# Kernel optimization log

Hardware: AMD Instinct MI355X
Metric: run time of the kernel (lower is better)

The kernel has to match this reference:

```python
import jax, jax.numpy as jnp
import numpy as np

NUM_HEADS = 8
LN_EPS = 1e-5


def setup_inputs() -> dict:
    key = jax.random.key(0)
    ks = jax.random.split(key, 5)
    B, C, H, W = 4, 256, 48, 48
    scale = 1.0 / np.sqrt(C)
    return {
        "x": jax.random.normal(ks[0], (B, C, H, W), dtype=jnp.float32),
        "Wq": jax.random.normal(ks[1], (C, C), dtype=jnp.float32) * scale,
        "Wk": jax.random.normal(ks[2], (C, C), dtype=jnp.float32) * scale,
        "Wv": jax.random.normal(ks[3], (C, C), dtype=jnp.float32) * scale,
        "Wo": jax.random.normal(ks[4], (C, C), dtype=jnp.float32) * scale,
        "gamma": jnp.ones((C,), dtype=jnp.float32),
        "beta": jnp.zeros((C,), dtype=jnp.float32),
    }


def reference(x, Wq, Wk, Wv, Wo, gamma, beta):
    B, C, H, W = x.shape
    hd = C // NUM_HEADS
    N = H * W
    xf = x.reshape(B, C, N)  # [B, C, N]
    # 1x1 conv (no bias) == channel matmul, then split heads: [B, h, d, N]
    def proj(Wm):
        return jnp.einsum('oc,bcn->bon', Wm, xf).reshape(B, NUM_HEADS, hd, N)
    q = proj(Wq)
    k = proj(Wk)
    v = proj(Wv)
    # scores[b,h,i,j] = sum_d q[b,h,d,i] k[b,h,d,j] / sqrt(hd)
    scores = jnp.einsum('bhdi,bhdj->bhij', q, k) / jnp.sqrt(jnp.float32(hd))
    attn = jax.nn.softmax(scores, axis=-1)  # [B, h, N, N]
    # attended[b,h,d,i] = sum_j v[b,h,d,j] attn[b,h,i,j]
    attended = jnp.einsum('bhdj,bhij->bhdi', v, attn).reshape(B, C, H, W)
    out = jnp.einsum('oc,bchw->bohw', Wo, attended) + x
    # LayerNorm over channels (applied in NHWC layout in original)
    mu = out.mean(axis=1, keepdims=True)
    var = out.var(axis=1, keepdims=True)
    out = (out - mu) * jax.lax.rsqrt(var + LN_EPS)
    out = out * gamma[None, :, None, None] + beta[None, :, None, None]
    return out
```

## Files before the change

kernel.cpp:

```cpp
#include <hip/hip_runtime.h>

#define DEVI __device__ __forceinline__

typedef __bf16 bf16x8 __attribute__((ext_vector_type(8)));
typedef float f32x4 __attribute__((ext_vector_type(4)));

#define QSCALE 0.25503488f

DEVI unsigned short bfbits(float f) {
  union { __bf16 h; unsigned short u; } x;
  x.h = (__bf16)f;
  return x.u;
}
DEVI unsigned packbf2(float a, float b) {
  return (unsigned)bfbits(a) | ((unsigned)bfbits(b) << 16);
}
DEVI float bflo(unsigned u) { return __uint_as_float(u << 16); }
DEVI float bfhi(unsigned u) { return __uint_as_float(u & 0xffff0000u); }

DEVI void gload16(const unsigned short* g, void* l) {
  __builtin_amdgcn_global_load_lds((__attribute__((address_space(1))) const unsigned*)g,
                                   (__attribute__((address_space(3))) unsigned*)l, 16, 0, 0);
}

__global__ __launch_bounds__(256) void k_prep_x(const float* __restrict__ x,
                                                unsigned short* __restrict__ xT) {
  __shared__ float tile[64][65];
  const int b = blockIdx.x, n0 = blockIdx.y * 64, c0 = blockIdx.z * 64;
  const int t = threadIdx.x, tn = t & 63, tg = t >> 6;
  const float* xp = x + ((size_t)b * 256 + c0) * 2304 + n0;
#pragma unroll
  for (int i = 0; i < 16; ++i) {
    const int c = tg * 16 + i;
    tile[c][tn] = xp[(size_t)c * 2304 + tn];
  }
  __syncthreads();
  unsigned short* op = xT + ((size_t)b * 2304 + n0) * 256 + c0;
#pragma unroll
  for (int i = 0; i < 16; ++i) {
    const int n = tg * 16 + i;
    op[(size_t)n * 256 + tn] = bfbits(tile[tn][n]);
  }
}

__global__ __launch_bounds__(256) void k_prep_w(const float* __restrict__ Wq,
                                                const float* __restrict__ Wk,
                                                const float* __restrict__ Wv,
                                                const float* __restrict__ Wo,
                                                unsigned short* __restrict__ dst) {
  const float* src = blockIdx.y == 0 ? Wq : blockIdx.y == 1 ? Wk : blockIdx.y == 2 ? Wv : Wo;
  unsigned short* d = dst + (size_t)blockIdx.y * 65536;
  const int i = (blockIdx.x * 256 + threadIdx.x) * 4;
  const float4 v = *(const float4*)(src + i);
  uint2 u;
  u.x = packbf2(v.x, v.y);
  u.y = packbf2(v.z, v.w);
  *(uint2*)(d + i) = u;
}

__global__ __launch_bounds__(256) void k_proj_qk(const unsigned short* __restrict__ xT,
                                                 const unsigned short* __restrict__ Wb,
                                                 unsigned short* __restrict__ qT,
                                                 unsigned short* __restrict__ kT) {
  const unsigned short* W = Wb + (blockIdx.z ? 65536 : 0);
  unsigned short* outp = blockIdx.z ? kT : qT;
  const float scale = blockIdx.z ? 1.0f : QSCALE;
  const int l = threadIdx.x & 63, w = threadIdx.x >> 6;
  const int lr = l & 15, lg = l >> 4;
  const int row0 = blockIdx.x * 128 + w * 32;
  const int col0 = blockIdx.y * 32;
  f32x4 acc[2][2];
#pragma unroll
  for (int i = 0; i < 2; ++i)
#pragma unroll
    for (int j = 0; j < 2; ++j) acc[i][j] = (f32x4){0.f, 0.f, 0.f, 0.f};
  for (int ks = 0; ks < 8; ++ks) {
    const int c = ks * 32 + lg * 8;
    bf16x8 a[2], bfr[2];
#pragma unroll
    for (int nt = 0; nt < 2; ++nt)
      a[nt] = *(const bf16x8*)(xT + (size_t)(row0 + nt * 16 + lr) * 256 + c);
#pragma unroll
    for (int ot = 0; ot < 2; ++ot)
      bfr[ot] = *(const bf16x8*)(W + (size_t)(col0 + ot * 16 + lr) * 256 + c);
#pragma unroll
    for (int nt = 0; nt < 2; ++nt)
#pragma unroll
      for (int ot = 0; ot < 2; ++ot)
        acc[nt][ot] = __builtin_amdgcn_mfma_f32_16x16x32_bf16(a[nt], bfr[ot], acc[nt][ot], 0, 0, 0);
  }
#pragma unroll
  for (int nt = 0; nt < 2; ++nt)
#pragma unroll
    for (int ot = 0; ot < 2; ++ot)
#pragma unroll
      for (int r = 0; r < 4; ++r) {
        const int n = row0 + nt * 16 + lg * 4 + r;
        const int o = col0 + ot * 16 + lr;
        outp[(size_t)n * 256 + o] = bfbits(acc[nt][ot][r] * scale);
      }
}

__global__ __launch_bounds__(256) void k_proj_v(const unsigned short* __restrict__ xT,
                                                const unsigned short* __restrict__ Wv,
                                                unsigned short* __restrict__ vN) {
  const int l = threadIdx.x & 63, w = threadIdx.x >> 6;
  const int lr = l & 15, lg = l >> 4;
  const int row0 = blockIdx.x * 64 + w * 16;
  const int col0 = blockIdx.y * 32;
  f32x4 acc[2];
  acc[0] = (f32x4){0.f, 0.f, 0.f, 0.f};
  acc[1] = (f32x4){0.f, 0.f, 0.f, 0.f};
  for (int ks = 0; ks < 8; ++ks) {
    const int c = ks * 32 + lg * 8;
    bf16x8 a, bfr[2];
    a = *(const bf16x8*)(Wv + (size_t)(row0 + lr) * 256 + c);
#pragma unroll
    for (int nt = 0; nt < 2; ++nt)
      bfr[nt] = *(const bf16x8*)(xT + (size_t)(col0 + nt * 16 + lr) * 256 + c);
#pragma unroll
    for (int nt = 0; nt < 2; ++nt)
      acc[nt] = __builtin_amdgcn_mfma_f32_16x16x32_bf16(a, bfr[nt], acc[nt], 0, 0, 0);
  }
  const int b = blockIdx.y / 72, nb = (blockIdx.y % 72) * 32;
#pragma unroll
  for (int nt = 0; nt < 2; ++nt)
#pragma unroll
    for (int r = 0; r < 4; ++r) {
      const int o = row0 + lg * 4 + r;
      const int n = nb + nt * 16 + lr;
      vN[(size_t)b * 589824 + (size_t)o * 2304 + n] = bfbits(acc[nt][r]);
    }
}

template <bool DIRECT>
__global__ __launch_bounds__(256) void k_attn(const unsigned short* __restrict__ qT,
                                              const unsigned short* __restrict__ kT,
                                              const unsigned short* __restrict__ vN,
                                              unsigned short* __restrict__ partO,
                                              float* __restrict__ partS,
                                              unsigned short* __restrict__ attT,
                                              int tpc) {
  __shared__ __align__(16) unsigned char sm[32768];
  const int l = threadIdx.x & 63, w = threadIdx.x >> 6;
  const int lr = l & 15, lg = l >> 4;
  const int bh = blockIdx.y, b = bh >> 3, h = bh & 7;
  const int i0 = blockIdx.x * 128 + w * 32;
  const int c = blockIdx.z, t0 = c * tpc;
  unsigned char* smw = sm + w * 4096;

  bf16x8 qf[2];
#pragma unroll
  for (int it = 0; it < 2; ++it)
    qf[it] = *(const bf16x8*)(qT + (size_t)(b * 2304 + i0 + it * 16 + lr) * 256 + h * 32 + lg * 8);

  bf16x8 ones;
#pragma unroll
  for (int e = 0; e < 8; ++e) ones[e] = (__bf16)1.0f;

  f32x4 oacc[2][2];
#pragma unroll
  for (int i = 0; i < 2; ++i)
#pragma unroll
    for (int j = 0; j < 2; ++j) oacc[i][j] = (f32x4){0.f, 0.f, 0.f, 0.f};
  f32x4 psum[2];
  psum[0] = (f32x4){0.f, 0.f, 0.f, 0.f};
  psum[1] = (f32x4){0.f, 0.f, 0.f, 0.f};

  const unsigned short* ksrc = kT + (size_t)(b * 2304 + l) * 256 + h * 32 + w * 8;
  const int vks = w >> 1;
  const int vlg = (w * 2 + (l >> 5)) & 3;
  const unsigned short* vsrc = vN + (size_t)(b * 256 + h * 32 + (l & 31)) * 2304 + vks * 32 + vlg * 8;
  const int kdst = 16384 + w * 1024;
  const int vdst = 24576 + w * 1024;

  gload16(ksrc + (size_t)t0 * 16384, sm + kdst);
  gload16(vsrc + t0 * 64, sm + vdst);
  __syncthreads();

  for (int tt = 0; tt < tpc; ++tt) {
    const int buf = tt & 1;
    if (tt < tpc - 1) {
      const int nbuf = (tt + 1) & 1;
      gload16(ksrc + (size_t)(t0 + tt + 1) * 16384, sm + kdst + nbuf * 4096);
      gload16(vsrc + (t0 + tt + 1) * 64, sm + vdst + nbuf * 4096);
    }

    const unsigned char* kb = sm + 16384 + buf * 4096;
    const unsigned char* vb = sm + 24576 + buf * 4096;

    bf16x8 kf[4];
#pragma unroll
    for (int jt = 0; jt < 4; ++jt)
      kf[jt] = *(const bf16x8*)(kb + lg * 1024 + (jt * 16 + lr) * 16);

    f32x4 s[4][2];
    const f32x4 zf = (f32x4){0.f, 0.f, 0.f, 0.f};
#pragma unroll
    for (int jt = 0; jt < 4; ++jt)
#pragma unroll
      for (int it = 0; it < 2; ++it)
        s[jt][it] = __builtin_amdgcn_mfma_f32_16x16x32_bf16(kf[jt], qf[it], zf, 0, 0, 0);

#pragma unroll
    for (int it = 0; it < 2; ++it) {
      const int iloc = it * 16 + lr;
      const unsigned swz = (unsigned)((iloc & 7) << 4);
      unsigned char* prow = smw + iloc * 128;
#pragma unroll
      for (int jt = 0; jt < 4; ++jt) {
        const float p0 = exp2f(s[jt][it][0]);
        const float p1 = exp2f(s[jt][it][1]);
        const float p2 = exp2f(s[jt][it][2]);
        const float p3 = exp2f(s[jt][it][3]);
        const unsigned jb = (unsigned)(jt * 32 + lg * 8);
        *(unsigned*)(prow + (jb ^ swz)) = packbf2(p0, p1);
        *(unsigned*)(prow + ((jb + 4) ^ swz)) = packbf2(p2, p3);
      }
    }

    bf16x8 vf[2][2], pf[2][2];
#pragma unroll
    for (int dt = 0; dt < 2; ++dt)
#pragma unroll
      for (int ks = 0; ks < 2; ++ks)
        vf[dt][ks] = *(const bf16x8*)(vb + ks * 2048 + lg * 512 + (dt * 16 + lr) * 16);
#pragma unroll
    for (int it = 0; it < 2; ++it) {
      const int iloc = it * 16 + lr;
      const unsigned swz = (unsigned)((iloc & 7) << 4);
#pragma unroll
      for (int ks = 0; ks < 2; ++ks)
        pf[it][ks] = *(const bf16x8*)(smw + iloc * 128 + ((unsigned)(ks * 64 + lg * 16) ^ swz));
    }
#pragma unroll
    for (int dt = 0; dt < 2; ++dt)
#pragma unroll
      for (int it = 0; it < 2; ++it) {
        oacc[dt][it] = __builtin_amdgcn_mfma_f32_16x16x32_bf16(vf[dt][0], pf[it][0], oacc[dt][it], 0, 0, 0);
        oacc[dt][it] = __builtin_amdgcn_mfma_f32_16x16x32_bf16(vf[dt][1], pf[it][1], oacc[dt][it], 0, 0, 0);
      }
#pragma unroll
    for (int it = 0; it < 2; ++it) {
      psum[it] = __builtin_amdgcn_mfma_f32_16x16x32_bf16(ones, pf[it][0], psum[it], 0, 0, 0);
      psum[it] = __builtin_amdgcn_mfma_f32_16x16x32_bf16(ones, pf[it][1], psum[it], 0, 0, 0);
    }
    __syncthreads();
  }

  if (DIRECT) {
#pragma unroll
    for (int it = 0; it < 2; ++it) {
      const float inv = 1.0f / psum[it][0];
      const int iloc = it * 16 + lr;
      unsigned char* orow = smw + iloc * 68;
#pragma unroll
      for (int dt = 0; dt < 2; ++dt) {
        const int d = dt * 16 + lg * 4;
        *(unsigned*)(orow + d * 2) = packbf2(oacc[dt][it][0] * inv, oacc[dt][it][1] * inv);
        *(unsigned*)(orow + d * 2 + 4) = packbf2(oacc[dt][it][2] * inv, oacc[dt][it][3] * inv);
      }
    }
    __syncthreads();
    unsigned* attu = (unsigned*)attT;
#pragma unroll
    for (int it2 = 0; it2 < 8; ++it2) {
      const int lin = it2 * 64 + l;
      const int row = lin >> 4, k = lin & 15;
      const unsigned u = *(const unsigned*)(smw + row * 68 + k * 4);
      attu[(size_t)(b * 2304 + i0 + row) * 128 + h * 16 + k] = u;
    }
  } else {
    const size_t pbase = ((size_t)(c * 32 + bh) * 2304 + i0) * 32;
#pragma unroll
    for (int it = 0; it < 2; ++it)
#pragma unroll
      for (int dt = 0; dt < 2; ++dt) {
        const size_t addr = pbase + (size_t)(it * 16 + lr) * 32 + dt * 16 + lg * 4;
        uint2 u;
        u.x = packbf2(oacc[dt][it][0], oacc[dt][it][1]);
        u.y = packbf2(oacc[dt][it][2], oacc[dt][it][3]);
        *(uint2*)(partO + addr) = u;
      }
    if (lg == 0) {
      const size_t sbase = (size_t)(c * 32 + bh) * 2304 + i0;
      partS[sbase + lr] = psum[0][0];
      partS[sbase + 16 + lr] = psum[1][0];
    }
  }
}

__global__ __launch_bounds__(256) void k_combine(const unsigned short* __restrict__ partO,
                                                 const float* __restrict__ partS,
                                                 unsigned short* __restrict__ attT,
                                                 int nc) {
  const int bid = blockIdx.x;
  const int bh = bid / 36, i0 = (bid % 36) * 64;
  const int b = bh >> 3, h = bh & 7;
  const int tid = threadIdx.x;
  const int dq = tid & 3, di = tid >> 2;
  const int i = i0 + di;

  float ssum = 0.f;
  for (int c = 0; c < nc; ++c) ssum += partS[(size_t)(c * 32 + bh) * 2304 + i];
  const float inv = 1.0f / ssum;

  float acc[8];
#pragma unroll
  for (int e = 0; e < 8; ++e) acc[e] = 0.f;
  for (int c = 0; c < nc; ++c) {
    const uint4 v = *(const uint4*)(partO + (((size_t)(c * 32 + bh) * 2304 + i) * 32 + dq * 8));
    acc[0] += bflo(v.x); acc[1] += bfhi(v.x);
    acc[2] += bflo(v.y); acc[3] += bfhi(v.y);
    acc[4] += bflo(v.z); acc[5] += bfhi(v.z);
    acc[6] += bflo(v.w); acc[7] += bfhi(v.w);
  }
  uint4 o;
  o.x = packbf2(acc[0] * inv, acc[1] * inv);
  o.y = packbf2(acc[2] * inv, acc[3] * inv);
  o.z = packbf2(acc[4] * inv, acc[5] * inv);
  o.w = packbf2(acc[6] * inv, acc[7] * inv);
  unsigned* attu = (unsigned*)attT;
  *(uint4*)(attu + (size_t)(b * 2304 + i) * 128 + h * 16 + dq * 4) = o;
}

__global__ __launch_bounds__(256) void k_out_ln(const unsigned short* __restrict__ Wo,
                                                const unsigned short* __restrict__ attT,
                                                const float* __restrict__ x,
                                                const float* __restrict__ gamma,
                                                const float* __restrict__ beta,
                                                float* __restrict__ out) {
  __shared__ float wsum[4][16], wsq[4][16], smean[16], srstd[16];
  const int l = threadIdx.x & 63, w = threadIdx.x >> 6;
  const int lr = l & 15, lg = l >> 4;
  const int b = blockIdx.x / 144;
  const int n0 = (blockIdx.x % 144) * 16;
  const int row0 = w * 64;
  const size_t bn0 = (size_t)b * 2304 + n0;

  f32x4 acc[4];
#pragma unroll
  for (int i = 0; i < 4; ++i) acc[i] = (f32x4){0.f, 0.f, 0.f, 0.f};
  for (int ks = 0; ks < 8; ++ks) {
    const int c = ks * 32 + lg * 8;
    bf16x8 a[4], bb;
#pragma unroll
    for (int rt = 0; rt < 4; ++rt)
      a[rt] = *(const bf16x8*)(Wo + (size_t)(row0 + rt * 16 + lr) * 256 + c);
    bb = *(const bf16x8*)(attT + (bn0 + lr) * 256 + c);
#pragma unroll
    for (int rt = 0; rt < 4; ++rt)
      acc[rt] = __builtin_amdgcn_mfma_f32_16x16x32_bf16(a[rt], bb, acc[rt], 0, 0, 0);
  }
  const float* xb = x + (size_t)b * 589824;
  float vals[4][4];
  float s0 = 0.f, q0 = 0.f;
#pragma unroll
  for (int rt = 0; rt < 4; ++rt)
#pragma unroll
    for (int r = 0; r < 4; ++r) {
      const int o = row0 + rt * 16 + lg * 4 + r;
      const int n = n0 + lr;
      const float vv = acc[rt][r] + xb[(size_t)o * 2304 + n];
      vals[rt][r] = vv;
      s0 += vv;
      q0 += vv * vv;
    }
  s0 += __shfl_xor(s0, 16); s0 += __shfl_xor(s0, 32);
  q0 += __shfl_xor(q0, 16); q0 += __shfl_xor(q0, 32);
  if (l < 16) {
    wsum[w][l] = s0;
    wsq[w][l] = q0;
  }
  __syncthreads();
  if (threadIdx.x < 16) {
    const int c16 = threadIdx.x;
    const float S = wsum[0][c16] + wsum[1][c16] + wsum[2][c16] + wsum[3][c16];
    const float Q = wsq[0][c16] + wsq[1][c16] + wsq[2][c16] + wsq[3][c16];
    const float mean = S * (1.0f / 256.0f);
    const float var = Q * (1.0f / 256.0f) - mean * mean;
    smean[c16] = mean;
    srstd[c16] = rsqrtf(var + 1e-5f);
  }
  __syncthreads();
  {
    const float mean = smean[lr];
    const float rstd = srstd[lr];
    const int n = n0 + lr;
#pragma unroll
    for (int rt = 0; rt < 4; ++rt)
#pragma unroll
      for (int r = 0; r < 4; ++r) {
        const int o = row0 + rt * 16 + lg * 4 + r;
        out[(size_t)b * 589824 + (size_t)o * 2304 + n] =
            (vals[rt][r] - mean) * rstd * gamma[o] + beta[o];
      }
  }
}

extern "C" void kernel_launch(void* const* d_in, const int* in_sizes, int n_in,
                              void* d_out, int out_size, void* d_ws, size_t ws_size,
                              hipStream_t stream) {
  (void)in_sizes; (void)n_in; (void)out_size;
  const float* x = (const float*)d_in[0];
  const float* Wq = (const float*)d_in[1];
  const float* Wk = (const float*)d_in[2];
  const float* Wv = (const float*)d_in[3];
  const float* Wo = (const float*)d_in[4];
  const float* gamma = (const float*)d_in[5];
  const float* beta = (const float*)d_in[6];
  float* out = (float*)d_out;
  char* ws = (char*)d_ws;
  unsigned short* attT = (unsigned short*)(ws);
  unsigned short* Wb = (unsigned short*)(ws + 4718592);
  unsigned short* qT = (unsigned short*)(ws + 5242880);
  unsigned short* kT = (unsigned short*)(ws + 9961472);
  unsigned short* vN = (unsigned short*)(ws + 14680064);
  unsigned short* xT = (unsigned short*)(ws + 19398656);

  const size_t base = 19398656;
  const size_t need4 = base + 4ull * (4718592 + 294912);
  const size_t need2 = base + 2ull * (4718592 + 294912);
  const int nc = (ws_size >= need4) ? 4 : (ws_size >= need2) ? 2 : 1;
  unsigned short* partO = (unsigned short*)(ws + base);
  float* partS = (float*)(ws + base + (size_t)nc * 4718592);

  k_prep_x<<<dim3(4, 36, 4), 256, 0, stream>>>(x, xT);
  k_prep_w<<<dim3(64, 4), 256, 0, stream>>>(Wq, Wk, Wv, Wo, Wb);
  k_proj_qk<<<dim3(72, 8, 2), 256, 0, stream>>>(xT, Wb, qT, kT);
  k_proj_v<<<dim3(4, 288), 256, 0, stream>>>(xT, Wb + 2 * 65536, vN);
  if (nc > 1) {
    k_attn<false><<<dim3(18, 32, nc), 256, 0, stream>>>(qT, kT, vN, partO, partS, attT, 36 / nc);
    k_combine<<<dim3(1152), 256, 0, stream>>>(partO, partS, attT, nc);
  } else {
    k_attn<true><<<dim3(18, 32, 1), 256, 0, stream>>>(qT, kT, vN, attT, (float*)attT, attT, 36);
  }
  k_out_ln<<<dim3(576), 256, 0, stream>>>(Wb + 3 * 65536, attT, x, gamma, beta, out);
}
```

Measured before the change: 193.6 us.

## Stage shared operands in swizzled LDS and use native exp2 in attention

Three projection/output kernels now stage the block-shared operand (W tile for q/k and v projections, attention tile for output projection) into XOR-swizzled LDS once, so waves stop re-reading it from global memory in the k-loop. The attention softmax switches to the hardware exp2 builtin, and the two 32-bit P stores are merged into one 64-bit LDS store. The cost is extra LDS use, a barrier per block, and slightly lower exp2 accuracy.

New measurement: 168.4 us. 13.0% less time.

```diff
diff --git a/kernel.cpp b/kernel.cpp
--- a/kernel.cpp
+++ b/kernel.cpp
@@ -6,6 +6,12 @@
 typedef float f32x4 __attribute__((ext_vector_type(4)));
 
 #define QSCALE 0.25503488f
+
+#if __has_builtin(__builtin_amdgcn_exp2f)
+#define EXP2(x) __builtin_amdgcn_exp2f(x)
+#else
+#define EXP2(x) __expf(0.69314718055994531f * (x))
+#endif
 
 DEVI unsigned short bfbits(float f) {
   union { __bf16 h; unsigned short u; } x;
@@ -62,6 +68,7 @@
                                                  const unsigned short* __restrict__ Wb,
                                                  unsigned short* __restrict__ qT,
                                                  unsigned short* __restrict__ kT) {
+  __shared__ __align__(16) unsigned char wlds[16384];
   const unsigned short* W = Wb + (blockIdx.z ? 65536 : 0);
   unsigned short* outp = blockIdx.z ? kT : qT;
   const float scale = blockIdx.z ? 1.0f : QSCALE;
@@ -69,6 +76,19 @@
   const int lr = l & 15, lg = l >> 4;
   const int row0 = blockIdx.x * 128 + w * 32;
   const int col0 = blockIdx.y * 32;
+  {
+    const int t = threadIdx.x;
+    const int row = t >> 3;
+    const int cj0 = (t & 7) * 4;
+#pragma unroll
+    for (int i = 0; i < 4; ++i) {
+      const int cj = cj0 + i;
+      const uint4 v = *(const uint4*)(W + (size_t)(col0 + row) * 256 + cj * 8);
+      *(uint4*)(wlds + row * 512 + ((cj * 16) ^ ((row & 7) << 4))) = v;
+    }
+  }
+  __syncthreads();
+
   f32x4 acc[2][2];
 #pragma unroll
   for (int i = 0; i < 2; ++i)
@@ -81,8 +101,10 @@
     for (int nt = 0; nt < 2; ++nt)
       a[nt] = *(const bf16x8*)(xT + (size_t)(row0 + nt * 16 + lr) * 256 + c);
 #pragma unroll
-    for (int ot = 0; ot < 2; ++ot)
-      bfr[ot] = *(const bf16x8*)(W + (size_t)(col0 + ot * 16 + lr) * 256 + c);
+    for (int ot = 0; ot < 2; ++ot) {
+      const int brow = ot * 16 + lr;
+      bfr[ot] = *(const bf16x8*)(wlds + brow * 512 + (((ks * 4 + lg) * 16) ^ ((brow & 7) << 4)));
+    }
 #pragma unroll
     for (int nt = 0; nt < 2; ++nt)
 #pragma unroll
@@ -104,17 +126,32 @@
 __global__ __launch_bounds__(256) void k_proj_v(const unsigned short* __restrict__ xT,
                                                 const unsigned short* __restrict__ Wv,
                                                 unsigned short* __restrict__ vN) {
+  __shared__ __align__(16) unsigned char wlds[32768];
   const int l = threadIdx.x & 63, w = threadIdx.x >> 6;
   const int lr = l & 15, lg = l >> 4;
-  const int row0 = blockIdx.x * 64 + w * 16;
+  const int rowbase = blockIdx.x * 64;
   const int col0 = blockIdx.y * 32;
+  {
+    const int t = threadIdx.x;
+    const int row = t >> 2;
+    const int cj0 = (t & 3) * 8;
+#pragma unroll
+    for (int i = 0; i < 8; ++i) {
+      const int cj = cj0 + i;
+      const uint4 v = *(const uint4*)(Wv + (size_t)(rowbase + row) * 256 + cj * 8);
+      *(uint4*)(wlds + row * 512 + ((cj * 16) ^ ((row & 7) << 4))) = v;
+    }
+  }
+  __syncthreads();
+
   f32x4 acc[2];
   acc[0] = (f32x4){0.f, 0.f, 0.f, 0.f};
   acc[1] = (f32x4){0.f, 0.f, 0.f, 0.f};
   for (int ks = 0; ks < 8; ++ks) {
     const int c = ks * 32 + lg * 8;
     bf16x8 a, bfr[2];
-    a = *(const bf16x8*)(Wv + (size_t)(row0 + lr) * 256 + c);
+    const int arow = w * 16 + lr;
+    a = *(const bf16x8*)(wlds + arow * 512 + (((ks * 4 + lg) * 16) ^ ((arow & 7) << 4)));
 #pragma unroll
     for (int nt = 0; nt < 2; ++nt)
       bfr[nt] = *(const bf16x8*)(xT + (size_t)(col0 + nt * 16 + lr) * 256 + c);
@@ -127,7 +164,7 @@
   for (int nt = 0; nt < 2; ++nt)
 #pragma unroll
     for (int r = 0; r < 4; ++r) {
-      const int o = row0 + lg * 4 + r;
+      const int o = rowbase + w * 16 + lg * 4 + r;
       const int n = nb + nt * 16 + lr;
       vN[(size_t)b * 589824 + (size_t)o * 2304 + n] = bfbits(acc[nt][r]);
     }
@@ -209,13 +246,15 @@
       unsigned char* prow = smw + iloc * 128;
 #pragma unroll
       for (int jt = 0; jt < 4; ++jt) {
-        const float p0 = exp2f(s[jt][it][0]);
-        const float p1 = exp2f(s[jt][it][1]);
-        const float p2 = exp2f(s[jt][it][2]);
-        const float p3 = exp2f(s[jt][it][3]);
+        const float p0 = EXP2(s[jt][it][0]);
+        const float p1 = EXP2(s[jt][it][1]);
+        const float p2 = EXP2(s[jt][it][2]);
+        const float p3 = EXP2(s[jt][it][3]);
         const unsigned jb = (unsigned)(jt * 32 + lg * 8);
-        *(unsigned*)(prow + (jb ^ swz)) = packbf2(p0, p1);
-        *(unsigned*)(prow + ((jb + 4) ^ swz)) = packbf2(p2, p3);
+        uint2 u;
+        u.x = packbf2(p0, p1);
+        u.y = packbf2(p2, p3);
+        *(uint2*)(prow + (jb ^ swz)) = u;
       }
     }
 
@@ -330,6 +369,7 @@
                                                 const float* __restrict__ gamma,
                                                 const float* __restrict__ beta,
                                                 float* __restrict__ out) {
+  __shared__ __align__(16) unsigned char alds[8192];
   __shared__ float wsum[4][16], wsq[4][16], smean[16], srstd[16];
   const int l = threadIdx.x & 63, w = threadIdx.x >> 6;
   const int lr = l & 15, lg = l >> 4;
@@ -337,6 +377,18 @@
   const int n0 = (blockIdx.x % 144) * 16;
   const int row0 = w * 64;
   const size_t bn0 = (size_t)b * 2304 + n0;
+  {
+    const int t = threadIdx.x;
+    const int row = t >> 4;
+    const int cj0 = (t & 15) * 2;
+#pragma unroll
+    for (int i = 0; i < 2; ++i) {
+      const int cj = cj0 + i;
+      const uint4 v = *(const uint4*)(attT + (bn0 + row) * 256 + cj * 8);
+      *(uint4*)(alds + row * 512 + ((cj * 16) ^ ((row & 7) << 4))) = v;
+    }
+  }
+  __syncthreads();
 
   f32x4 acc[4];
 #pragma unroll
@@ -347,7 +399,7 @@
 #pragma unroll
     for (int rt = 0; rt < 4; ++rt)
       a[rt] = *(const bf16x8*)(Wo + (size_t)(row0 + rt * 16 + lr) * 256 + c);
-    bb = *(const bf16x8*)(attT + (bn0 + lr) * 256 + c);
+    bb = *(const bf16x8*)(alds + lr * 512 + (((ks * 4 + lg) * 16) ^ ((lr & 7) << 4)));
 #pragma unroll
     for (int rt = 0; rt < 4; ++rt)
       acc[rt] = __builtin_amdgcn_mfma_f32_16x16x32_bf16(a[rt], bb, acc[rt], 0, 0, 0);
```
